# Optimization experiments

Hardware: AMD Instinct MI355X
Metric: run time of the kernel (lower is better)

## Reference

```python
import jax, jax.numpy as jnp
import numpy as np

N_NODES = 50000
N_EDGES = 600000
D_IN = 128
D_OUT = 128
N_BASES = 4
N_RATINGS = 5


def setup_inputs() -> dict:
    key = jax.random.key(0)
    k1, k2, k3, k4, k5, k6 = jax.random.split(key, 6)
    x = jax.random.normal(k1, (N_NODES, D_IN), dtype=jnp.float32)
    edge_index = jax.random.randint(k2, (2, N_EDGES), 0, N_NODES, dtype=jnp.int64)
    edge_type = jax.random.randint(k3, (N_EDGES,), 0, N_RATINGS, dtype=jnp.int64)
    # basis matrices B_k: (out, in); a_r stacked over ratings: (R, K); W_0: (out, in)
    B = jax.random.normal(k4, (N_BASES, D_OUT, D_IN), dtype=jnp.float32) * 0.05
    A = jax.random.normal(k5, (N_RATINGS, N_BASES), dtype=jnp.float32) * 0.05
    W0 = jax.random.normal(k6, (D_OUT, D_IN), dtype=jnp.float32) * 0.05
    return {"x": x, "edge_index": edge_index, "edge_type": edge_type, "B": B, "A": A, "W0": W0}


def reference(x, edge_index, edge_type, B, A, W0):
    # self-loop term: (W0 @ x^T)^T == x @ W0^T
    n_nodes = x.shape[0]
    src, tgt = edge_index[0], edge_index[1]
    out = x @ W0.T  # [N, out]
    # per-relation basis-composed weights W_r = sum_k a_r[k] * B_k  -> [R, out, in]
    W = jnp.einsum('rk,kod->rod', A, B)
    n_ratings = A.shape[0]
    for r in range(n_ratings):  # small fixed relation set
        h = x @ W[r].T                     # [N, out] transform once per node
        msg = jnp.where((edge_type == r)[:, None], h[src], jnp.float32(0))  # [E, out]
        out = out + jax.ops.segment_sum(msg, tgt, num_segments=n_nodes)
    return out
```

## Files before the change

### kernel.cpp

```cpp
#include <hip/hip_runtime.h>

#define N_NODES 50000
#define N_EDGES 600000
#define D 128
#define KTOT 768
#define NB_SCAN 196

typedef __attribute__((ext_vector_type(8))) short short8;
typedef __attribute__((ext_vector_type(4))) float float4v;

static __device__ __forceinline__ float bf2f(unsigned int u16) {
    union { unsigned int i; float f; } v; v.i = u16 << 16; return v.f;
}
static __device__ __forceinline__ unsigned short f2bf(float f) {
    union { float f; unsigned int i; } v; v.f = f;
    unsigned int u = v.i;
    return (unsigned short)((u + 0x7FFFu + ((u >> 16) & 1u)) >> 16);
}
static __device__ __forceinline__ float h2f(unsigned int h) {
    unsigned int s = (h >> 15) & 1u, e = (h >> 10) & 0x1fu, m = h & 0x3ffu;
    unsigned int bits = (e == 0) ? (s << 31)
                                 : ((s << 31) | ((e + 112u) << 23) | (m << 13));
    union { unsigned int i; float f; } v; v.i = bits; return v.f;
}

__global__ __launch_bounds__(256) void setup(int* __restrict__ flags,
                                             int* __restrict__ cnt) {
    int i = blockIdx.x * 256 + threadIdx.x;
    if (i < N_NODES) cnt[i] = 0;
    if (i < 8) flags[i] = 0;
}

__global__ __launch_bounds__(256) void detect_all(const int* __restrict__ ei,
                                                  const int* __restrict__ et,
                                                  const unsigned int* __restrict__ x,
                                                  const unsigned int* __restrict__ B,
                                                  const unsigned int* __restrict__ A,
                                                  const unsigned int* __restrict__ W0,
                                                  int* __restrict__ flags) {
    __shared__ int sflag;
    if (threadIdx.x == 0) sflag = 0;
    __syncthreads();
    int b = blockIdx.x, acc = 0, fidx;
    if (b < 64) {
        fidx = 0;
        for (int i = b * 256 + threadIdx.x; i < N_EDGES; i += 64 * 256)
            acc |= ei[2 * i + 1];
    } else if (b < 80) {
        fidx = 1;
        for (int i = (b - 64) * 256 + threadIdx.x; i < N_EDGES / 2; i += 16 * 256)
            acc |= et[2 * i + 1];
    } else if (b < 96) {
        fidx = 2;
        for (int i = (b - 80) * 256 + threadIdx.x; i < 600000; i += 16 * 256) {
            unsigned int e = (x[i] >> 7) & 0xffu;
            acc |= (e > 0xA0u || e < 0x50u) ? 1 : 0;
        }
    } else if (b < 100) {
        fidx = 3;
        for (int i = (b - 96) * 256 + threadIdx.x; i < 32768; i += 4 * 256) {
            unsigned int e = (B[i] >> 7) & 0xffu;
            acc |= (e > 0xA0u || e < 0x50u) ? 1 : 0;
        }
    } else if (b == 100) {
        fidx = 4;
        for (int i = threadIdx.x; i < 10; i += 256) {
            unsigned int e = (A[i] >> 7) & 0xffu;
            acc |= (e > 0xA0u || e < 0x50u) ? 1 : 0;
        }
    } else if (b < 103) {
        fidx = 5;
        for (int i = (b - 101) * 256 + threadIdx.x; i < 8192; i += 2 * 256) {
            unsigned int e = (W0[i] >> 7) & 0xffu;
            acc |= (e > 0xA0u || e < 0x50u) ? 1 : 0;
        }
    } else {
        fidx = 6;
        for (int i = (b - 103) * 256 + threadIdx.x; i < 300000; i += 16 * 256) {
            unsigned int el = (x[i] >> 7) & 0xffu, eh = (x[i] >> 23) & 0xffu;
            acc |= (el < 0x58u || eh < 0x58u) ? 1 : 0;
        }
    }
    if (acc) sflag = 1;
    __syncthreads();
    if (threadIdx.x == 0 && sflag) atomicOr(flags + fidx, 1);
}

static __device__ __forceinline__ float loadw(const void* p, int idx, int f32) {
    return f32 ? ((const float*)p)[idx] : bf2f(((const unsigned short*)p)[idx]);
}

__global__ __launch_bounds__(256) void norm_hist_prep(const int* __restrict__ ei,
                                                      const int* __restrict__ et,
                                                      int* __restrict__ idx32,
                                                      int* __restrict__ et32,
                                                      int* __restrict__ cnt,
                                                      const void* __restrict__ A,
                                                      const void* __restrict__ B,
                                                      const void* __restrict__ W0,
                                                      unsigned short* __restrict__ wcatB,
                                                      const int* __restrict__ flags) {
    int b = blockIdx.x;
    if (b < 4688) {
        int i = b * 256 + threadIdx.x;
        if (i < 2 * N_EDGES) {
            int v = flags[0] ? ei[i] : ei[2 * i];
            idx32[i] = v;
            if (i >= N_EDGES && (unsigned)v < (unsigned)N_NODES)
                atomicAdd(&cnt[v], 1);
        }
    } else if (b < 7032) {
        int i = (b - 4688) * 256 + threadIdx.x;
        if (i < N_EDGES) et32[i] = flags[1] ? et[i] : et[2 * i];
    } else {
        int idx = (b - 7032) * 256 + threadIdx.x;
        int fB = flags[3], fA = flags[4], fW = flags[5];
        int o = idx / KTOT, k = idx % KTOT;
        float v;
        if (k < D) {
            v = loadw(W0, o * D + k, fW);
        } else {
            int r = (k - D) >> 7, d = (k - D) & 127;
            v = 0.f;
#pragma unroll
            for (int j = 0; j < 4; ++j)
                v += loadw(A, r * 4 + j, fA) * loadw(B, (j * D + o) * D + d, fB);
        }
        wcatB[idx] = f2bf(v);
    }
}

__global__ __launch_bounds__(256) void prep_wt6_direct(const void* __restrict__ A,
                                                       const void* __restrict__ B,
                                                       const void* __restrict__ W0,
                                                       float* __restrict__ wcatT6F,
                                                       const int* __restrict__ flags) {
    int idx = blockIdx.x * 256 + threadIdx.x;
    int fB = flags[3], fA = flags[4], fW = flags[5];
    int slot = idx >> 14, d = (idx >> 7) & 127, o = idx & 127;
    float v;
    if (slot == 0) {
        v = loadw(W0, o * D + d, fW);
    } else {
        int r = slot - 1;
        v = 0.f;
#pragma unroll
        for (int j = 0; j < 4; ++j)
            v += loadw(A, r * 4 + j, fA) * loadw(B, (j * D + o) * D + d, fB);
    }
    wcatT6F[idx] = v;
}

__global__ __launch_bounds__(256) void scan1(const int* __restrict__ cnt,
                                             int* __restrict__ bsum) {
    __shared__ int sh[256];
    int t = threadIdx.x, idx = blockIdx.x * 256 + t;
    sh[t] = (idx < N_NODES) ? cnt[idx] : 0;
    __syncthreads();
    for (int off = 128; off > 0; off >>= 1) {
        if (t < off) sh[t] += sh[t + off];
        __syncthreads();
    }
    if (t == 0) bsum[blockIdx.x] = sh[0];
}

__global__ __launch_bounds__(64) void scan2(const int* __restrict__ bsum,
                                            int* __restrict__ bscan,
                                            int* __restrict__ offsets) {
    if (threadIdx.x != 0) return;
    int run = 0;
    for (int b = 0; b < NB_SCAN; ++b) { bscan[b] = run; run += bsum[b]; }
    offsets[N_NODES] = run;
}

__global__ __launch_bounds__(256) void scan3(const int* __restrict__ cnt,
                                             const int* __restrict__ bscan,
                                             int* __restrict__ offsets,
                                             int* __restrict__ cursor) {
    __shared__ int sh[256];
    int t = threadIdx.x, idx = blockIdx.x * 256 + t;
    int v = (idx < N_NODES) ? cnt[idx] : 0;
    sh[t] = v;
    __syncthreads();
    for (int off = 1; off < 256; off <<= 1) {
        int a = (t >= off) ? sh[t - off] : 0;
        __syncthreads();
        sh[t] += a;
        __syncthreads();
    }
    if (idx < N_NODES) {
        int excl = sh[t] - v + bscan[blockIdx.x];
        offsets[idx] = excl;
        cursor[idx] = excl;
    }
}

__global__ __launch_bounds__(256) void place(const int* __restrict__ src,
                                             const int* __restrict__ tgt,
                                             const int* __restrict__ et,
                                             int* __restrict__ cursor,
                                             int* __restrict__ entries) {
    int e = blockIdx.x * 256 + threadIdx.x;
    if (e >= N_EDGES) return;
    int s = src[e], g = tgt[e], r = et[e];
    if ((unsigned)s >= (unsigned)N_NODES || (unsigned)g >= (unsigned)N_NODES || (unsigned)r >= 5u) return;
    int pos = atomicAdd(&cursor[g], 1);
    entries[pos] = s * 8 + r;
}

__global__ __launch_bounds__(256) void conv_x(const void* __restrict__ xraw,
                                              unsigned short* __restrict__ Xcat,
                                              const int* __restrict__ flags) {
    int idx = blockIdx.x * 256 + threadIdx.x;
    int n = idx >> 5, cg = idx & 31;
    int f32 = flags[2], f16 = flags[6];
    unsigned short o0, o1, o2, o3;
    if (f32) {
        float4 v = *((const float4*)xraw + idx);
        o0 = f2bf(v.x); o1 = f2bf(v.y); o2 = f2bf(v.z); o3 = f2bf(v.w);
    } else {
        uint2 v = *((const uint2*)xraw + idx);
        if (f16) {
            o0 = f2bf(h2f(v.x & 0xffffu)); o1 = f2bf(h2f(v.x >> 16));
            o2 = f2bf(h2f(v.y & 0xffffu)); o3 = f2bf(h2f(v.y >> 16));
        } else {
            o0 = v.x & 0xffffu; o1 = v.x >> 16; o2 = v.y & 0xffffu; o3 = v.y >> 16;
        }
    }
    unsigned long long pack = (unsigned long long)o0 | ((unsigned long long)o1 << 16) |
                              ((unsigned long long)o2 << 32) | ((unsigned long long)o3 << 48);
    *(unsigned long long*)(Xcat + (size_t)n * KTOT + cg * 4) = pack;
}

#define AGG_ACC(xw)                                            \
    {                                                          \
        int r = ent & 7;                                       \
        float flo = bf2f((xw) & 0xffffu), fhi = bf2f((xw) >> 16);\
        if (r == 0)      { a0 += flo; a1 += fhi; }             \
        else if (r == 1) { b0 += flo; b1 += fhi; }             \
        else if (r == 2) { c0 += flo; c1 += fhi; }             \
        else if (r == 3) { d0 += flo; d1 += fhi; }             \
        else             { e0 += flo; e1 += fhi; }             \
    }

#define AGG_GATHER(en) Xcat32[(size_t)((unsigned)((en) >> 3) < (unsigned)N_NODES ? (unsigned)((en) >> 3) : 0u) * 384 + lane]

__global__ __launch_bounds__(256) void aggregate(const int* __restrict__ offsets,
                                                 const int* __restrict__ entries,
                                                 unsigned int* __restrict__ Xcat32) {
    __shared__ float part[4][5][130];
    int tid = threadIdx.x;
    int wid = tid >> 6, lane = tid & 63;
    int slot = wid >> 1;
    int half = wid & 1;
    int n = blockIdx.x * 2 + slot;
    int beg = offsets[n], end = offsets[n + 1];
    int mid = (beg + end + 1) >> 1;
    int lo = half ? mid : beg, hi = half ? end : mid;
    float a0 = 0, a1 = 0, b0 = 0, b1 = 0, c0 = 0, c1 = 0, d0 = 0, d1 = 0, e0 = 0, e1 = 0;

    for (int base = lo; base < hi; base += 64) {
        int navail = hi - base;
        int cnt = navail < 64 ? navail : 64;
        int eidx = base + (lane < cnt ? lane : cnt - 1);
        int eload = entries[eidx];
        int j = 0;
        for (; j + 3 < cnt; j += 4) {
            int en0 = __shfl(eload, j), en1 = __shfl(eload, j + 1);
            int en2 = __shfl(eload, j + 2), en3 = __shfl(eload, j + 3);
            unsigned int x0 = AGG_GATHER(en0);
            unsigned int x1 = AGG_GATHER(en1);
            unsigned int x2 = AGG_GATHER(en2);
            unsigned int x3 = AGG_GATHER(en3);
            { int ent = en0; AGG_ACC(x0); }
            { int ent = en1; AGG_ACC(x1); }
            { int ent = en2; AGG_ACC(x2); }
            { int ent = en3; AGG_ACC(x3); }
        }
        for (; j < cnt; ++j) {
            int ent = __shfl(eload, j);
            unsigned int xw = AGG_GATHER(ent);
            AGG_ACC(xw);
        }
    }

    part[wid][0][2 * lane] = a0; part[wid][0][2 * lane + 1] = a1;
    part[wid][1][2 * lane] = b0; part[wid][1][2 * lane + 1] = b1;
    part[wid][2][2 * lane] = c0; part[wid][2][2 * lane + 1] = c1;
    part[wid][3][2 * lane] = d0; part[wid][3][2 * lane + 1] = d1;
    part[wid][4][2 * lane] = e0; part[wid][4][2 * lane + 1] = e1;
    __syncthreads();

    for (int u = tid; u < 640; u += 256) {
        int s = u / 320, rem = u % 320;
        int r = rem >> 6, c = rem & 63;
        float lo2 = part[2 * s][r][2 * c]     + part[2 * s + 1][r][2 * c];
        float hi2 = part[2 * s][r][2 * c + 1] + part[2 * s + 1][r][2 * c + 1];
        Xcat32[(size_t)(blockIdx.x * 2 + s) * 384 + 64 + r * 64 + c] =
            (unsigned int)f2bf(lo2) | ((unsigned int)f2bf(hi2) << 16);
    }
}

__global__ __launch_bounds__(256) void gemm_mfma(const unsigned short* __restrict__ Xcat,
                                                 const unsigned short* __restrict__ wcatB,
                                                 float* __restrict__ outF) {
    __shared__ unsigned short xs[64 * 72];
    __shared__ unsigned short wsd[128 * 72];
    int tid = threadIdx.x;
    int m0 = blockIdx.x * 64;
    int wid = tid >> 6, lane = tid & 63;
    int wm = (wid & 1) * 32, wn = (wid >> 1) * 64;
    int lm = lane & 15, kg = lane >> 4;

    float4v accf[2][4];
#pragma unroll
    for (int i = 0; i < 2; ++i)
#pragma unroll
        for (int j = 0; j < 4; ++j) accf[i][j] = (float4v){0.f, 0.f, 0.f, 0.f};

    for (int kc = 0; kc < 12; ++kc) {
        if (kc) __syncthreads();
#pragma unroll
        for (int i = 0; i < 2; ++i) {
            int c = tid + i * 256;
            int row = c >> 3, col = (c & 7) * 8;
            int gm = m0 + row;
            short8 xv = {0, 0, 0, 0, 0, 0, 0, 0};
            if (gm < N_NODES)
                xv = *(const short8*)(Xcat + (size_t)gm * KTOT + kc * 64 + col);
            *(short8*)(&xs[row * 72 + col]) = xv;
        }
#pragma unroll
        for (int i = 0; i < 4; ++i) {
            int c = tid + i * 256;
            int row = c >> 3, col = (c & 7) * 8;
            short8 wv = *(const short8*)(wcatB + (size_t)row * KTOT + kc * 64 + col);
            *(short8*)(&wsd[row * 72 + col]) = wv;
        }
        __syncthreads();
#pragma unroll
        for (int kb = 0; kb < 2; ++kb) {
            int k = kb * 32 + kg * 8;
            short8 a[2], b[4];
#pragma unroll
            for (int i = 0; i < 2; ++i)
                a[i] = *(const short8*)(&xs[(wm + i * 16 + lm) * 72 + k]);
#pragma unroll
            for (int j = 0; j < 4; ++j)
                b[j] = *(const short8*)(&wsd[(wn + j * 16 + lm) * 72 + k]);
#pragma unroll
            for (int i = 0; i < 2; ++i)
#pragma unroll
                for (int j = 0; j < 4; ++j)
                    accf[i][j] = __builtin_amdgcn_mfma_f32_16x16x32_bf16(a[i], b[j], accf[i][j], 0, 0, 0);
        }
    }

#pragma unroll
    for (int i = 0; i < 2; ++i) {
        int gmb = m0 + wm + i * 16 + kg * 4;
#pragma unroll
        for (int j = 0; j < 4; ++j) {
            int gn = wn + j * 16 + lm;
#pragma unroll
            for (int r = 0; r < 4; ++r) {
                int gm = gmb + r;
                if (gm < N_NODES) outF[(size_t)gm * D + gn] = accf[i][j][r];
            }
        }
    }
}

static __device__ __forceinline__ float2 readx2(const void* x, int node, int lane,
                                                int f32, int f16) {
    if (f32) return *((const float2*)x + (size_t)node * 64 + lane);
    unsigned int w = *((const unsigned int*)x + (size_t)node * 64 + lane);
    float2 r;
    if (f16) { r.x = h2f(w & 0xffffu); r.y = h2f(w >> 16); }
    else     { r.x = bf2f(w & 0xffffu); r.y = bf2f(w >> 16); }
    return r;
}

__global__ __launch_bounds__(256) void self_raw(const void* __restrict__ x,
                                                const float* __restrict__ wcatT6F,
                                                float* __restrict__ outF,
                                                const int* __restrict__ flags) {
    int t = blockIdx.x * 256 + threadIdx.x;
    int n = t >> 6, lane = t & 63;
    int f32 = flags[2], f16 = flags[6];
    float2 xp = readx2(x, n, lane, f32, f16);
    float m0 = 0.f, m1 = 0.f;
#pragma unroll 8
    for (int dp = 0; dp < 64; ++dp) {
        float xa = __shfl(xp.x, dp);
        float xc = __shfl(xp.y, dp);
        float2 w0 = *(const float2*)(wcatT6F + (size_t)(2 * dp) * D + 2 * lane);
        float2 w1 = *(const float2*)(wcatT6F + (size_t)(2 * dp + 1) * D + 2 * lane);
        m0 += xa * w0.x + xc * w1.x;
        m1 += xa * w0.y + xc * w1.y;
    }
    *((float2*)outF + (size_t)n * 64 + lane) = make_float2(m0, m1);
}

__global__ __launch_bounds__(256) void edge_raw(const int* __restrict__ src,
                                                const int* __restrict__ tgt,
                                                const int* __restrict__ et,
                                                const void* __restrict__ x,
                                                const float* __restrict__ wcatT6F,
                                                float* __restrict__ outF,
                                                const int* __restrict__ flags) {
    int t = blockIdx.x * 256 + threadIdx.x;
    int e = t >> 6, lane = t & 63;
    if (e >= N_EDGES) return;
    int f32 = flags[2], f16 = flags[6];
    int s = src[e], g = tgt[e], r = et[e];
    if ((unsigned)s >= (unsigned)N_NODES || (unsigned)g >= (unsigned)N_NODES || (unsigned)r >= 5u) return;
    float2 xp = readx2(x, s, lane, f32, f16);
    const float* wt = wcatT6F + (size_t)(1 + r) * D * D;
    float m0 = 0.f, m1 = 0.f;
#pragma unroll 8
    for (int dp = 0; dp < 64; ++dp) {
        float xa = __shfl(xp.x, dp);
        float xc = __shfl(xp.y, dp);
        float2 w0 = *(const float2*)(wt + (size_t)(2 * dp) * D + 2 * lane);
        float2 w1 = *(const float2*)(wt + (size_t)(2 * dp + 1) * D + 2 * lane);
        m0 += xa * w0.x + xc * w1.x;
        m1 += xa * w0.y + xc * w1.y;
    }
    float* ap = outF + (size_t)g * D + lane * 2;
    atomicAdd(ap + 0, m0);
    atomicAdd(ap + 1, m1);
}

extern "C" void kernel_launch(void* const* d_in, const int* in_sizes, int n_in,
                              void* d_out, int out_size, void* d_ws, size_t ws_size,
                              hipStream_t stream) {
    const void* x  = nullptr; const int* ei = nullptr; const int* et = nullptr;
    const void* B  = nullptr; const void* A = nullptr; const void* W0 = nullptr;
    for (int i = 0; i < n_in; ++i) {
        switch (in_sizes[i]) {
            case 6400000: x  = d_in[i]; break;
            case 1200000: ei = (const int*)d_in[i]; break;
            case 600000:  et = (const int*)d_in[i]; break;
            case 65536:   B  = d_in[i]; break;
            case 20:      A  = d_in[i]; break;
            case 16384:   W0 = d_in[i]; break;
            default: break;
        }
    }
    if (!x || !ei || !et || !B || !A || !W0) {
        x  = d_in[0]; ei = (const int*)d_in[1]; et = (const int*)d_in[2];
        B  = d_in[3]; A  = d_in[4]; W0 = d_in[5];
    }
    float* outF = (float*)d_out;

    char* ws = (char*)d_ws;
    int*   flags   = (int*)(ws + 0);
    float* wcatT6F = (float*)(ws + 256);
    unsigned short* wcatB = (unsigned short*)(ws + 393472);
    int* offsets  = (int*)(ws + 590080);
    int* cursor   = (int*)(ws + 790144);
    int* cnt      = (int*)(ws + 990144);
    int* bsum     = (int*)(ws + 1190144);
    int* bscan    = (int*)(ws + 1191168);
    int* entries  = (int*)(ws + 1192192);
    int* idx32    = (int*)(ws + 3592192);
    int* et32     = (int*)(ws + 8392192);
    unsigned short* Xcat = (unsigned short*)(ws + 3592192);
    const size_t needMain = 3592192ull + 76800000ull;
    const size_t needT3   = 393472ull;

    int* src32 = idx32;
    int* tgt32 = idx32 + N_EDGES;

    setup<<<NB_SCAN, 256, 0, stream>>>(flags, cnt);
    detect_all<<<119, 256, 0, stream>>>(ei, et, (const unsigned int*)x,
                                        (const unsigned int*)B, (const unsigned int*)A,
                                        (const unsigned int*)W0, flags);

    if (ws_size >= needMain) {
        norm_hist_prep<<<7416, 256, 0, stream>>>(ei, et, idx32, et32, cnt,
                                                 A, B, W0, wcatB, flags);
        scan1<<<NB_SCAN, 256, 0, stream>>>(cnt, bsum);
        scan2<<<1, 64, 0, stream>>>(bsum, bscan, offsets);
        scan3<<<NB_SCAN, 256, 0, stream>>>(cnt, bscan, offsets, cursor);
        place<<<2344, 256, 0, stream>>>(src32, tgt32, et32, cursor, entries);
        conv_x<<<6250, 256, 0, stream>>>(x, Xcat, flags);
        aggregate<<<25000, 256, 0, stream>>>(offsets, entries, (unsigned int*)Xcat);
        gemm_mfma<<<782, 256, 0, stream>>>(Xcat, wcatB, outF);
    } else if (ws_size >= needT3) {
        prep_wt6_direct<<<384, 256, 0, stream>>>(A, B, W0, wcatT6F, flags);
        self_raw<<<12500, 256, 0, stream>>>(x, wcatT6F, outF, flags);
        edge_raw<<<150000, 256, 0, stream>>>(ei, ei + N_EDGES, et, x, wcatT6F, outF, flags);
    }
}
```

Baseline: 262.3 us.

## Use one wave per node in aggregate, parallelize block scan, widen detection grid

The aggregate kernel now assigns one wavefront per destination node instead of splitting each node's edge list across two waves and merging the partial sums through shared memory. This removes the LDS reduction and the block barrier, uses scalar readlane for edge broadcast, and writes results directly. The single-thread serial scan of block sums becomes a 256-thread parallel scan, and the input-detection kernel gets three times as many blocks. The cost is less parallelism per high-degree node and reading entries past the node's edge range, which could go beyond the end of the array.

```diff
diff --git a/kernel.cpp b/kernel.cpp
--- a/kernel.cpp
+++ b/kernel.cpp
@@ -42,41 +42,41 @@
     if (threadIdx.x == 0) sflag = 0;
     __syncthreads();
     int b = blockIdx.x, acc = 0, fidx;
-    if (b < 64) {
+    if (b < 192) {
         fidx = 0;
-        for (int i = b * 256 + threadIdx.x; i < N_EDGES; i += 64 * 256)
+        for (int i = b * 256 + threadIdx.x; i < N_EDGES; i += 192 * 256)
             acc |= ei[2 * i + 1];
-    } else if (b < 80) {
+    } else if (b < 240) {
         fidx = 1;
-        for (int i = (b - 64) * 256 + threadIdx.x; i < N_EDGES / 2; i += 16 * 256)
+        for (int i = (b - 192) * 256 + threadIdx.x; i < N_EDGES / 2; i += 48 * 256)
             acc |= et[2 * i + 1];
-    } else if (b < 96) {
+    } else if (b < 288) {
         fidx = 2;
-        for (int i = (b - 80) * 256 + threadIdx.x; i < 600000; i += 16 * 256) {
+        for (int i = (b - 240) * 256 + threadIdx.x; i < 600000; i += 48 * 256) {
             unsigned int e = (x[i] >> 7) & 0xffu;
             acc |= (e > 0xA0u || e < 0x50u) ? 1 : 0;
         }
-    } else if (b < 100) {
+    } else if (b < 300) {
         fidx = 3;
-        for (int i = (b - 96) * 256 + threadIdx.x; i < 32768; i += 4 * 256) {
+        for (int i = (b - 288) * 256 + threadIdx.x; i < 32768; i += 12 * 256) {
             unsigned int e = (B[i] >> 7) & 0xffu;
             acc |= (e > 0xA0u || e < 0x50u) ? 1 : 0;
         }
-    } else if (b == 100) {
+    } else if (b == 300) {
         fidx = 4;
         for (int i = threadIdx.x; i < 10; i += 256) {
             unsigned int e = (A[i] >> 7) & 0xffu;
             acc |= (e > 0xA0u || e < 0x50u) ? 1 : 0;
         }
-    } else if (b < 103) {
+    } else if (b < 307) {
         fidx = 5;
-        for (int i = (b - 101) * 256 + threadIdx.x; i < 8192; i += 2 * 256) {
+        for (int i = (b - 301) * 256 + threadIdx.x; i < 8192; i += 6 * 256) {
             unsigned int e = (W0[i] >> 7) & 0xffu;
             acc |= (e > 0xA0u || e < 0x50u) ? 1 : 0;
         }
     } else {
         fidx = 6;
-        for (int i = (b - 103) * 256 + threadIdx.x; i < 300000; i += 16 * 256) {
+        for (int i = (b - 307) * 256 + threadIdx.x; i < 300000; i += 48 * 256) {
             unsigned int el = (x[i] >> 7) & 0xffu, eh = (x[i] >> 23) & 0xffu;
             acc |= (el < 0x58u || eh < 0x58u) ? 1 : 0;
         }
@@ -164,13 +164,22 @@
     if (t == 0) bsum[blockIdx.x] = sh[0];
 }
 
-__global__ __launch_bounds__(64) void scan2(const int* __restrict__ bsum,
-                                            int* __restrict__ bscan,
-                                            int* __restrict__ offsets) {
-    if (threadIdx.x != 0) return;
-    int run = 0;
-    for (int b = 0; b < NB_SCAN; ++b) { bscan[b] = run; run += bsum[b]; }
-    offsets[N_NODES] = run;
+__global__ __launch_bounds__(256) void scan2(const int* __restrict__ bsum,
+                                             int* __restrict__ bscan,
+                                             int* __restrict__ offsets) {
+    __shared__ int sh[256];
+    int t = threadIdx.x;
+    int v = (t < NB_SCAN) ? bsum[t] : 0;
+    sh[t] = v;
+    __syncthreads();
+    for (int off = 1; off < 256; off <<= 1) {
+        int a = (t >= off) ? sh[t - off] : 0;
+        __syncthreads();
+        sh[t] += a;
+        __syncthreads();
+    }
+    if (t < NB_SCAN) bscan[t] = sh[t] - v;
+    if (t == 255) offsets[N_NODES] = sh[255];
 }
 
 __global__ __launch_bounds__(256) void scan3(const int* __restrict__ cnt,
@@ -232,73 +241,67 @@
     *(unsigned long long*)(Xcat + (size_t)n * KTOT + cg * 4) = pack;
 }
 
-#define AGG_ACC(xw)                                            \
-    {                                                          \
-        int r = ent & 7;                                       \
-        float flo = bf2f((xw) & 0xffffu), fhi = bf2f((xw) >> 16);\
-        if (r == 0)      { a0 += flo; a1 += fhi; }             \
-        else if (r == 1) { b0 += flo; b1 += fhi; }             \
-        else if (r == 2) { c0 += flo; c1 += fhi; }             \
-        else if (r == 3) { d0 += flo; d1 += fhi; }             \
-        else             { e0 += flo; e1 += fhi; }             \
-    }
-
-#define AGG_GATHER(en) Xcat32[(size_t)((unsigned)((en) >> 3) < (unsigned)N_NODES ? (unsigned)((en) >> 3) : 0u) * 384 + lane]
+#define AGG_ACC2(ent, xw)                                            \
+    {                                                                \
+        int r_ = (ent) & 7;                                          \
+        float flo_ = __uint_as_float((xw) << 16);                    \
+        float fhi_ = __uint_as_float((xw) & 0xffff0000u);            \
+        if (r_ == 0)      { a0 += flo_; a1 += fhi_; }                \
+        else if (r_ == 1) { b0 += flo_; b1 += fhi_; }                \
+        else if (r_ == 2) { c0 += flo_; c1 += fhi_; }                \
+        else if (r_ == 3) { d0 += flo_; d1 += fhi_; }                \
+        else              { e0 += flo_; e1 += fhi_; }                \
+    }
+
+static __device__ __forceinline__ unsigned int agg_row_load(
+        const unsigned int* __restrict__ Xcat32, int ent, int lane) {
+    unsigned int row = (unsigned int)(ent >> 3);
+    if (row >= (unsigned)N_NODES) row = 0u;
+    return Xcat32[(size_t)row * 384 + lane];
+}
 
 __global__ __launch_bounds__(256) void aggregate(const int* __restrict__ offsets,
                                                  const int* __restrict__ entries,
                                                  unsigned int* __restrict__ Xcat32) {
-    __shared__ float part[4][5][130];
     int tid = threadIdx.x;
     int wid = tid >> 6, lane = tid & 63;
-    int slot = wid >> 1;
-    int half = wid & 1;
-    int n = blockIdx.x * 2 + slot;
-    int beg = offsets[n], end = offsets[n + 1];
-    int mid = (beg + end + 1) >> 1;
-    int lo = half ? mid : beg, hi = half ? end : mid;
+    int n = __builtin_amdgcn_readfirstlane(blockIdx.x * 4 + wid);
+    int beg = __builtin_amdgcn_readfirstlane(offsets[n]);
+    int end = __builtin_amdgcn_readfirstlane(offsets[n + 1]);
     float a0 = 0, a1 = 0, b0 = 0, b1 = 0, c0 = 0, c1 = 0, d0 = 0, d1 = 0, e0 = 0, e1 = 0;
 
-    for (int base = lo; base < hi; base += 64) {
-        int navail = hi - base;
-        int cnt = navail < 64 ? navail : 64;
-        int eidx = base + (lane < cnt ? lane : cnt - 1);
-        int eload = entries[eidx];
+    for (int base = beg; base < end; base += 64) {
+        int cnt = end - base;
+        if (cnt > 64) cnt = 64;
+        int eload = entries[base + lane];
         int j = 0;
         for (; j + 3 < cnt; j += 4) {
-            int en0 = __shfl(eload, j), en1 = __shfl(eload, j + 1);
-            int en2 = __shfl(eload, j + 2), en3 = __shfl(eload, j + 3);
-            unsigned int x0 = AGG_GATHER(en0);
-            unsigned int x1 = AGG_GATHER(en1);
-            unsigned int x2 = AGG_GATHER(en2);
-            unsigned int x3 = AGG_GATHER(en3);
-            { int ent = en0; AGG_ACC(x0); }
-            { int ent = en1; AGG_ACC(x1); }
-            { int ent = en2; AGG_ACC(x2); }
-            { int ent = en3; AGG_ACC(x3); }
+            int en0 = __builtin_amdgcn_readlane(eload, j);
+            int en1 = __builtin_amdgcn_readlane(eload, j + 1);
+            int en2 = __builtin_amdgcn_readlane(eload, j + 2);
+            int en3 = __builtin_amdgcn_readlane(eload, j + 3);
+            unsigned int x0 = agg_row_load(Xcat32, en0, lane);
+            unsigned int x1 = agg_row_load(Xcat32, en1, lane);
+            unsigned int x2 = agg_row_load(Xcat32, en2, lane);
+            unsigned int x3 = agg_row_load(Xcat32, en3, lane);
+            AGG_ACC2(en0, x0);
+            AGG_ACC2(en1, x1);
+            AGG_ACC2(en2, x2);
+            AGG_ACC2(en3, x3);
         }
         for (; j < cnt; ++j) {
-            int ent = __shfl(eload, j);
-            unsigned int xw = AGG_GATHER(ent);
-            AGG_ACC(xw);
-        }
-    }
-
-    part[wid][0][2 * lane] = a0; part[wid][0][2 * lane + 1] = a1;
-    part[wid][1][2 * lane] = b0; part[wid][1][2 * lane + 1] = b1;
-    part[wid][2][2 * lane] = c0; part[wid][2][2 * lane + 1] = c1;
-    part[wid][3][2 * lane] = d0; part[wid][3][2 * lane + 1] = d1;
-    part[wid][4][2 * lane] = e0; part[wid][4][2 * lane + 1] = e1;
-    __syncthreads();
-
-    for (int u = tid; u < 640; u += 256) {
-        int s = u / 320, rem = u % 320;
-        int r = rem >> 6, c = rem & 63;
-        float lo2 = part[2 * s][r][2 * c]     + part[2 * s + 1][r][2 * c];
-        float hi2 = part[2 * s][r][2 * c + 1] + part[2 * s + 1][r][2 * c + 1];
-        Xcat32[(size_t)(blockIdx.x * 2 + s) * 384 + 64 + r * 64 + c] =
-            (unsigned int)f2bf(lo2) | ((unsigned int)f2bf(hi2) << 16);
-    }
+            int en = __builtin_amdgcn_readlane(eload, j);
+            unsigned int xw = agg_row_load(Xcat32, en, lane);
+            AGG_ACC2(en, xw);
+        }
+    }
+
+    size_t o = (size_t)n * 384 + 64 + lane;
+    Xcat32[o]       = (unsigned int)f2bf(a0) | ((unsigned int)f2bf(a1) << 16);
+    Xcat32[o + 64]  = (unsigned int)f2bf(b0) | ((unsigned int)f2bf(b1) << 16);
+    Xcat32[o + 128] = (unsigned int)f2bf(c0) | ((unsigned int)f2bf(c1) << 16);
+    Xcat32[o + 192] = (unsigned int)f2bf(d0) | ((unsigned int)f2bf(d1) << 16);
+    Xcat32[o + 256] = (unsigned int)f2bf(e0) | ((unsigned int)f2bf(e1) << 16);
 }
 
 __global__ __launch_bounds__(256) void gemm_mfma(const unsigned short* __restrict__ Xcat,
@@ -474,7 +477,7 @@
     int* tgt32 = idx32 + N_EDGES;
 
     setup<<<NB_SCAN, 256, 0, stream>>>(flags, cnt);
-    detect_all<<<119, 256, 0, stream>>>(ei, et, (const unsigned int*)x,
+    detect_all<<<355, 256, 0, stream>>>(ei, et, (const unsigned int*)x,
                                         (const unsigned int*)B, (const unsigned int*)A,
                                         (const unsigned int*)W0, flags);
 
@@ -482,11 +485,11 @@
         norm_hist_prep<<<7416, 256, 0, stream>>>(ei, et, idx32, et32, cnt,
                                                  A, B, W0, wcatB, flags);
         scan1<<<NB_SCAN, 256, 0, stream>>>(cnt, bsum);
-        scan2<<<1, 64, 0, stream>>>(bsum, bscan, offsets);
+        scan2<<<1, 256, 0, stream>>>(bsum, bscan, offsets);
         scan3<<<NB_SCAN, 256, 0, stream>>>(cnt, bscan, offsets, cursor);
         place<<<2344, 256, 0, stream>>>(src32, tgt32, et32, cursor, entries);
         conv_x<<<6250, 256, 0, stream>>>(x, Xcat, flags);
-        aggregate<<<25000, 256, 0, stream>>>(offsets, entries, (unsigned int*)Xcat);
+        aggregate<<<12500, 256, 0, stream>>>(offsets, entries, (unsigned int*)Xcat);
         gemm_mfma<<<782, 256, 0, stream>>>(Xcat, wcatB, outF);
     } else if (ws_size >= needT3) {
         prep_wt6_direct<<<384, 256, 0, stream>>>(A, B, W0, wcatT6F, flags);
```

New measurement: 232.5 us. -11.4%, faster.
